# Performance work log

Hardware: AMD Instinct MI355X
Metric: run time of the kernel (lower is better)

The kernel has to match this reference:

```python
import jax, jax.numpy as jnp
import numpy as np

B, T, E, H = 8, 1024, 1024, 16
D = E // H  # head_dim = 64
MAX_OFFSET = 0.5


def setup_inputs() -> dict:
    key = jax.random.key(0)
    ks = jax.random.split(key, 12)
    s = 0.02
    return {
        "query": jax.random.normal(ks[0], (B, T, E), jnp.float32),
        "key_": jax.random.normal(ks[1], (B, T, E), jnp.float32),
        "value": jax.random.normal(ks[2], (B, T, E), jnp.float32),
        "Wq": jax.random.normal(ks[3], (E, E), jnp.float32) * s,
        "bq": jnp.zeros((E,), jnp.float32),
        "Wk": jax.random.normal(ks[4], (E, E), jnp.float32) * s,
        "bk": jnp.zeros((E,), jnp.float32),
        "Wv": jax.random.normal(ks[5], (E, E), jnp.float32) * s,
        "bv": jnp.zeros((E,), jnp.float32),
        "Wo": jax.random.normal(ks[6], (E, E), jnp.float32) * s,
        "bo": jnp.zeros((E,), jnp.float32),
        "bias_table": jax.random.normal(ks[7], (2 * T - 1, H), jnp.float32) * s,
        "offset": jax.random.normal(ks[8], (1,), jnp.float32) * 0.1,
    }


def _temporal_bias(bias_table, offset):
    # relative position index: [T, T] in [0, 2T-2]
    coords = jnp.arange(T)
    rel = (coords[:, None] - coords[None, :]) + (T - 1)
    bounded = jnp.tanh(offset) * MAX_OFFSET  # scalar (shape (1,))
    adj = jnp.clip(rel.astype(jnp.float32) + bounded, 0.0, 2.0 * T - 2.0)
    lo = jnp.floor(adj).astype(jnp.int32)
    hi = jnp.ceil(adj).astype(jnp.int32)
    w = adj - lo.astype(jnp.float32)  # [T, T]
    lo_val = bias_table[lo]  # [T, T, H]
    hi_val = bias_table[hi]  # [T, T, H]
    bias = lo_val * (1.0 - w[..., None]) + hi_val * w[..., None]
    # -> [1, H, T, T]
    return jnp.transpose(bias, (2, 0, 1))[None]


def reference(query, key_, value, Wq, bq, Wk, bk, Wv, bv, Wo, bo, bias_table, offset):
    scale = D ** -0.5
    # torch Linear: x @ W.T + b
    q = (jnp.einsum('bte,fe->btf', query, Wq) + bq).reshape(B, T, H, D).transpose(0, 2, 1, 3)
    k = (jnp.einsum('bte,fe->btf', key_, Wk) + bk).reshape(B, T, H, D).transpose(0, 2, 1, 3)
    v = (jnp.einsum('bte,fe->btf', value, Wv) + bv).reshape(B, T, H, D).transpose(0, 2, 1, 3)
    scores = jnp.einsum('bhqd,bhkd->bhqk', q, k) * scale  # [B, H, T, T]
    scores = scores + _temporal_bias(bias_table, offset)
    attn = jax.nn.softmax(scores, axis=-1)
    out = jnp.einsum('bhqk,bhkd->bhqd', attn, v)  # [B, H, T, D]
    out = out.transpose(0, 2, 1, 3).reshape(B, T, E)
    return jnp.einsum('bte,fe->btf', out, Wo) + bo
```

## Files before the change

### kernel.cpp

```cpp
#include <hip/hip_runtime.h>
#include <hip/hip_bf16.h>
#include <stdint.h>

#define B_ 8
#define T_ 1024
#define E_ 1024
#define H_ 16
#define D_ 64
#define NREL 2047

using bf16 = __hip_bfloat16;
typedef __attribute__((ext_vector_type(8))) short bhalf8;
typedef __attribute__((ext_vector_type(4))) float f32x4;

typedef __attribute__((address_space(3))) uint32_t lds32_t;
typedef const __attribute__((address_space(1))) uint32_t glb32_t;
__device__ __forceinline__ void gld_lds16(const bf16* g, bf16* l) {
  __builtin_amdgcn_global_load_lds((glb32_t*)(const void*)g, (lds32_t*)(void*)l, 16, 0, 0);
}

__device__ __forceinline__ bhalf8 cvt8(const float4 a, const float4 b) {
  bf16 t[8];
  t[0] = __float2bfloat16(a.x); t[1] = __float2bfloat16(a.y);
  t[2] = __float2bfloat16(a.z); t[3] = __float2bfloat16(a.w);
  t[4] = __float2bfloat16(b.x); t[5] = __float2bfloat16(b.y);
  t[6] = __float2bfloat16(b.z); t[7] = __float2bfloat16(b.w);
  return *(const bhalf8*)t;
}

__global__ __launch_bounds__(256) void cvt_w4(const float* __restrict__ Wq,
                                              const float* __restrict__ Wk,
                                              const float* __restrict__ Wv,
                                              const float* __restrict__ Wo,
                                              bf16* __restrict__ d) {
  const int z = blockIdx.y;
  const float* s = (z == 0) ? Wq : (z == 1) ? Wk : (z == 2) ? Wv : Wo;
  const int i = (blockIdx.x * 256 + threadIdx.x) * 8;
  const float4 a = *(const float4*)(s + i);
  const float4 b = *(const float4*)(s + i + 4);
  *(bhalf8*)(d + (size_t)z * E_ * E_ + i) = cvt8(a, b);
}

__global__ void bias_pre(const float* __restrict__ table, const float* __restrict__ offset,
                         float* __restrict__ db) {
  const int idx = blockIdx.x * 256 + threadIdx.x;
  if (idx >= NREL * H_) return;
  const int r = idx >> 4;
  const int h = idx & 15;
  const float bounded = tanhf(offset[0]) * 0.5f;
  float adj = (float)r + bounded;
  adj = fminf(fmaxf(adj, 0.f), 2046.f);
  const int lo = (int)floorf(adj);
  const int hi = (int)ceilf(adj);
  const float wgt = adj - (float)lo;
  const float v = table[lo * H_ + h] * (1.f - wgt) + table[hi * H_ + h] * wgt;
  db[h * NREL + r] = v * 1.4426950408889634f;
}

__global__ __launch_bounds__(256, 3) void gemm_qkv(const float* __restrict__ Xq,
                                                   const float* __restrict__ Xk,
                                                   const float* __restrict__ Xv,
                                                   const bf16* __restrict__ Wc,
                                                   const float* __restrict__ bqp,
                                                   const float* __restrict__ bkp,
                                                   const float* __restrict__ bvp,
                                                   bf16* __restrict__ dst) {
  __shared__ bf16 As[2 * 128 * 32];
  __shared__ bf16 Bs[2 * 128 * 32];
  const int tid = threadIdx.x;
  const int lane = tid & 63;
  const int w = tid >> 6;
  const int quad = lane >> 4;
  const int l15 = lane & 15;
  const int m0 = blockIdx.x * 128;
  const int n0 = blockIdx.y * 128;
  const int z = blockIdx.z;
  const float* A = (z == 0) ? Xq : ((z == 1) ? Xk : Xv);
  const float* bias = (z == 0) ? bqp : ((z == 1) ? bkp : bvp);
  const bf16* W = Wc + (size_t)z * E_ * E_;
  bf16* out = dst + (size_t)z * B_ * T_ * D_ * H_;
  const int wm = (w >> 1) * 64;
  const int wn = (w & 1) * 64;

  const f32x4 zero4 = {0.f, 0.f, 0.f, 0.f};
  f32x4 acc[4][4];
#pragma unroll
  for (int i = 0; i < 4; ++i)
#pragma unroll
    for (int j = 0; j < 4; ++j) acc[i][j] = zero4;

  const int srow = w * 32 + (lane >> 2);
  const int scol = (lane & 3) * 8;
  const float* Ag = A + (size_t)(m0 + srow) * E_ + scol;
  const bf16* Wg = W + (size_t)(n0 + srow) * E_ + scol;
  const int sidx = w * 1024 + lane * 8;

  float4 p0 = *(const float4*)(Ag);
  float4 p1 = *(const float4*)(Ag + 4);
  float4 p2 = *(const float4*)(Ag + (size_t)16 * E_);
  float4 p3 = *(const float4*)(Ag + (size_t)16 * E_ + 4);
  *(bhalf8*)(As + sidx) = cvt8(p0, p1);
  *(bhalf8*)(As + sidx + 512) = cvt8(p2, p3);
  gld_lds16(Wg, Bs + sidx);
  gld_lds16(Wg + (size_t)16 * E_, Bs + sidx + 512);
  p0 = *(const float4*)(Ag + 32);
  p1 = *(const float4*)(Ag + 36);
  p2 = *(const float4*)(Ag + (size_t)16 * E_ + 32);
  p3 = *(const float4*)(Ag + (size_t)16 * E_ + 36);
  __syncthreads();

  for (int kt = 0; kt < 32; ++kt) {
    const int cur = (kt & 1) * 4096;
    bhalf8 af[4], bfr[4];
#pragma unroll
    for (int t2 = 0; t2 < 4; ++t2) {
      af[t2] = *(const bhalf8*)(As + cur + (wm + t2 * 16 + l15) * 32 + quad * 8);
      bfr[t2] = *(const bhalf8*)(Bs + cur + (wn + t2 * 16 + l15) * 32 + quad * 8);
    }
    if (kt < 31) {
      const int nxt = 4096 - cur;
      const int kc = (kt + 1) * 32;
      gld_lds16(Wg + kc, Bs + nxt + sidx);
      gld_lds16(Wg + (size_t)16 * E_ + kc, Bs + nxt + sidx + 512);
      *(bhalf8*)(As + nxt + sidx) = cvt8(p0, p1);
      *(bhalf8*)(As + nxt + sidx + 512) = cvt8(p2, p3);
      if (kt < 30) {
        const int kc2 = kc + 32;
        p0 = *(const float4*)(Ag + kc2);
        p1 = *(const float4*)(Ag + kc2 + 4);
        p2 = *(const float4*)(Ag + (size_t)16 * E_ + kc2);
        p3 = *(const float4*)(Ag + (size_t)16 * E_ + kc2 + 4);
      }
    }
#pragma unroll
    for (int mt = 0; mt < 4; ++mt)
#pragma unroll
      for (int nt = 0; nt < 4; ++nt)
        acc[mt][nt] = __builtin_amdgcn_mfma_f32_16x16x32_bf16(af[mt], bfr[nt], acc[mt][nt], 0, 0, 0);
    __syncthreads();
  }

#pragma unroll
  for (int mt = 0; mt < 4; ++mt) {
#pragma unroll
    for (int nt = 0; nt < 4; ++nt) {
      const int n = n0 + wn + nt * 16 + l15;
      const float bv = bias[n];
#pragma unroll
      for (int r = 0; r < 4; ++r) {
        const int m = m0 + wm + mt * 16 + quad * 4 + r;
        const float v = acc[mt][nt][r] + bv;
        const int bb = m >> 10, tq = m & 1023, hh = n >> 6, d = n & 63;
        out[(((size_t)bb * H_ + hh) * T_ + tq) * D_ + d] = __float2bfloat16(v);
      }
    }
  }
}

template <int SCATTER, int F32OUT>
__global__ __launch_bounds__(256) void gemm_bt(const bf16* __restrict__ A,
                                               const bf16* __restrict__ W,
                                               const float* __restrict__ bias,
                                               void* __restrict__ dst_) {
  __shared__ bf16 As[2 * 128 * 32];
  __shared__ bf16 Bs[2 * 128 * 32];
  const int tid = threadIdx.x;
  const int lane = tid & 63;
  const int w = tid >> 6;
  const int quad = lane >> 4;
  const int l15 = lane & 15;
  const int m0 = blockIdx.x * 128;
  const int n0 = blockIdx.y * 128;
  const int wm = (w >> 1) * 64;
  const int wn = (w & 1) * 64;

  const f32x4 zero4 = {0.f, 0.f, 0.f, 0.f};
  f32x4 acc[4][4];
#pragma unroll
  for (int i = 0; i < 4; ++i)
#pragma unroll
    for (int j = 0; j < 4; ++j) acc[i][j] = zero4;

  const int srow0 = w * 32 + (lane >> 2);
  const int scol = (lane & 3) * 8;
  const bf16* Ag = A + (size_t)(m0 + srow0) * E_ + scol;
  const bf16* Wg = W + (size_t)(n0 + srow0) * E_ + scol;
  const int sidx = w * 1024 + lane * 8;

  gld_lds16(Ag, As + sidx);
  gld_lds16(Ag + (size_t)16 * E_, As + sidx + 512);
  gld_lds16(Wg, Bs + sidx);
  gld_lds16(Wg + (size_t)16 * E_, Bs + sidx + 512);
  __syncthreads();

  for (int kt = 0; kt < 32; ++kt) {
    const int cur = (kt & 1) * 4096;
    bhalf8 af[4], bfr[4];
#pragma unroll
    for (int t = 0; t < 4; ++t) {
      af[t] = *(const bhalf8*)(As + cur + (wm + t * 16 + l15) * 32 + quad * 8);
      bfr[t] = *(const bhalf8*)(Bs + cur + (wn + t * 16 + l15) * 32 + quad * 8);
    }
    if (kt < 31) {
      const int nxt = 4096 - cur;
      const int kc = (kt + 1) * 32;
      gld_lds16(Ag + kc, As + nxt + sidx);
      gld_lds16(Ag + (size_t)16 * E_ + kc, As + nxt + sidx + 512);
      gld_lds16(Wg + kc, Bs + nxt + sidx);
      gld_lds16(Wg + (size_t)16 * E_ + kc, Bs + nxt + sidx + 512);
    }
#pragma unroll
    for (int mt = 0; mt < 4; ++mt)
#pragma unroll
      for (int nt = 0; nt < 4; ++nt)
        acc[mt][nt] = __builtin_amdgcn_mfma_f32_16x16x32_bf16(af[mt], bfr[nt], acc[mt][nt], 0, 0, 0);
    __syncthreads();
  }

#pragma unroll
  for (int mt = 0; mt < 4; ++mt) {
#pragma unroll
    for (int nt = 0; nt < 4; ++nt) {
      const int n = n0 + wn + nt * 16 + l15;
      const float bv = bias[n];
#pragma unroll
      for (int r = 0; r < 4; ++r) {
        const int m = m0 + wm + mt * 16 + quad * 4 + r;
        const float v = acc[mt][nt][r] + bv;
        if (SCATTER) {
          const int bb = m >> 10, t = m & 1023, hh = n >> 6, d = n & 63;
          ((bf16*)dst_)[(((size_t)bb * H_ + hh) * T_ + t) * D_ + d] = __float2bfloat16(v);
        } else if (F32OUT) {
          ((float*)dst_)[(size_t)m * E_ + n] = v;
        } else {
          ((bf16*)dst_)[(size_t)m * E_ + n] = __float2bfloat16(v);
        }
      }
    }
  }
}

__device__ __forceinline__ int ps_off(int row, int colbyte) {
  return row * 128 + (colbyte ^ ((row & 7) << 4));
}

__global__ __launch_bounds__(256, 4) void attn_kernel(const bf16* __restrict__ Q,
                                                      const bf16* __restrict__ K,
                                                      const bf16* __restrict__ V,
                                                      const float* __restrict__ db,
                                                      bf16* __restrict__ xout) {
  const int tid = threadIdx.x;
  const int lane = tid & 63;
  const int w = tid >> 6;
  const int quad = lane >> 4;
  const int l15 = lane & 15;
  const int bh = blockIdx.x;
  const int h = bh & 15;
  const int b = bh >> 4;
  const int q0 = blockIdx.y * 128;

  __shared__ bf16 Vt[64][72];
  __shared__ __align__(16) bf16 Ps[4][32 * 64];
  __shared__ float dbs[1152];

  const size_t base = (size_t)bh * T_ * D_;
  const bf16* Qp = Q + base;
  const bf16* Kp = K + base;
  const bf16* Vp = V + base;
  const float* dbh = db + h * NREL;

  for (int t = tid; t < 1151; t += 256) dbs[t] = dbh[q0 + t];

  const int qw = q0 + w * 32;
  bhalf8 aq[2][2];
#pragma unroll
  for (int mt = 0; mt < 2; ++mt)
#pragma unroll
    for (int ks = 0; ks < 2; ++ks)
      aq[mt][ks] = *(const bhalf8*)(Qp + (size_t)(qw + mt * 16 + l15) * D_ + ks * 32 + quad * 8);

  const f32x4 zero4 = {0.f, 0.f, 0.f, 0.f};
  f32x4 o[2][4];
#pragma unroll
  for (int mt = 0; mt < 2; ++mt)
#pragma unroll
    for (int nt = 0; nt < 4; ++nt) o[mt][nt] = zero4;
  float mrow[2] = {-1e30f, -1e30f};
  float lrow[2] = {0.f, 0.f};

  const int vrow0 = tid >> 3;
  const int vc8 = (tid & 7) * 8;
  bhalf8 vreg[2];
  vreg[0] = *(const bhalf8*)(Vp + (size_t)vrow0 * D_ + vc8);
  vreg[1] = *(const bhalf8*)(Vp + (size_t)(vrow0 + 32) * D_ + vc8);

  char* const psw = (char*)&Ps[w][0];

  for (int it = 0; it < 16; ++it) {
    const int kb = it * 64;
    bhalf8 bk[4][2];
#pragma unroll
    for (int nt = 0; nt < 4; ++nt) {
      const bf16* kr = Kp + (size_t)(kb + nt * 16 + l15) * D_ + quad * 8;
      bk[nt][0] = *(const bhalf8*)kr;
      bk[nt][1] = *(const bhalf8*)(kr + 32);
    }

    __syncthreads();
#pragma unroll
    for (int s = 0; s < 2; ++s) {
      const int row = vrow0 + s * 32;
      const bf16* vp = (const bf16*)&vreg[s];
      const int kvp = (row + vc8) & 63;
#pragma unroll
      for (int j = 0; j < 8; ++j) Vt[vc8 + j][kvp] = vp[j];
    }
    __syncthreads();
    if (it < 15) {
      const int kb2 = kb + 64;
      vreg[0] = *(const bhalf8*)(Vp + (size_t)(kb2 + vrow0) * D_ + vc8);
      vreg[1] = *(const bhalf8*)(Vp + (size_t)(kb2 + vrow0 + 32) * D_ + vc8);
    }

    f32x4 s4[2][4];
    __builtin_amdgcn_s_setprio(1);
#pragma unroll
    for (int nt = 0; nt < 4; ++nt) {
#pragma unroll
      for (int mt = 0; mt < 2; ++mt) {
        f32x4 a = zero4;
        a = __builtin_amdgcn_mfma_f32_16x16x32_bf16(bk[nt][0], aq[mt][0], a, 0, 0, 0);
        a = __builtin_amdgcn_mfma_f32_16x16x32_bf16(bk[nt][1], aq[mt][1], a, 0, 0, 0);
        s4[mt][nt] = a;
      }
    }
    __builtin_amdgcn_s_setprio(0);

#pragma unroll
    for (int mt = 0; mt < 2; ++mt) {
      const int ib = w * 32 + mt * 16 + l15 + 1023 - kb;
      float mnt[4];
#pragma unroll
      for (int nt = 0; nt < 4; ++nt) {
#pragma unroll
        for (int r = 0; r < 4; ++r) {
          const float sv = s4[mt][nt][r] * 0.18033688011112042f + dbs[ib - nt * 16 - quad * 4 - r];
          s4[mt][nt][r] = sv;
        }
        mnt[nt] = fmaxf(fmaxf(s4[mt][nt][0], s4[mt][nt][1]),
                        fmaxf(s4[mt][nt][2], s4[mt][nt][3]));
      }
      float tmx = fmaxf(fmaxf(mnt[0], mnt[1]), fmaxf(mnt[2], mnt[3]));
      tmx = fmaxf(tmx, __shfl_xor(tmx, 16, 64));
      tmx = fmaxf(tmx, __shfl_xor(tmx, 32, 64));
      if (!__all(tmx - mrow[mt] <= 11.0f)) {
        const float mnew = fmaxf(mrow[mt], tmx);
        const float alpha = __builtin_amdgcn_exp2f(mrow[mt] - mnew);
        mrow[mt] = mnew;
        lrow[mt] *= alpha;
#pragma unroll
        for (int nt = 0; nt < 4; ++nt) o[mt][nt] *= alpha;
      }
      const float mcur = mrow[mt];
      float psum[4];
#pragma unroll
      for (int nt = 0; nt < 4; ++nt) {
        float p0 = __builtin_amdgcn_exp2f(s4[mt][nt][0] - mcur);
        float p1 = __builtin_amdgcn_exp2f(s4[mt][nt][1] - mcur);
        float p2 = __builtin_amdgcn_exp2f(s4[mt][nt][2] - mcur);
        float p3 = __builtin_amdgcn_exp2f(s4[mt][nt][3] - mcur);
        s4[mt][nt][0] = p0; s4[mt][nt][1] = p1;
        s4[mt][nt][2] = p2; s4[mt][nt][3] = p3;
        psum[nt] = (p0 + p1) + (p2 + p3);
      }
      float sum = (psum[0] + psum[1]) + (psum[2] + psum[3]);
      sum += __shfl_xor(sum, 16, 64);
      sum += __shfl_xor(sum, 32, 64);
      lrow[mt] += sum;

#pragma unroll
      for (int nt = 0; nt < 4; ++nt) {
        alignas(8) bf16 t4[4];
#pragma unroll
        for (int r = 0; r < 4; ++r) t4[r] = __float2bfloat16(s4[mt][nt][r]);
        *(uint2*)(psw + ps_off(mt * 16 + l15, nt * 32 + quad * 8)) = *(const uint2*)t4;
      }
    }

    bhalf8 pb[2][2];
#pragma unroll
    for (int mt = 0; mt < 2; ++mt)
#pragma unroll
      for (int ks = 0; ks < 2; ++ks)
        pb[mt][ks] = *(const bhalf8*)(psw + ps_off(mt * 16 + l15, ks * 64 + quad * 16));
    const int rot = (l15 >> 3);
    __builtin_amdgcn_s_setprio(1);
#pragma unroll
    for (int nt = 0; nt < 4; ++nt) {
      const int drow = nt * 16 + l15;
#pragma unroll
      for (int ks = 0; ks < 2; ++ks) {
        const int gp = (4 * ks + quad + 2 * nt + rot) & 7;
        const bhalf8 vb = *(const bhalf8*)&Vt[drow][gp * 8];
#pragma unroll
        for (int mt = 0; mt < 2; ++mt)
          o[mt][nt] = __builtin_amdgcn_mfma_f32_16x16x32_bf16(vb, pb[mt][ks], o[mt][nt], 0, 0, 0);
      }
    }
    __builtin_amdgcn_s_setprio(0);
  }

#pragma unroll
  for (int mt = 0; mt < 2; ++mt) {
    const float inv = 1.f / lrow[mt];
#pragma unroll
    for (int nt = 0; nt < 4; ++nt) {
      alignas(8) bf16 t4[4];
#pragma unroll
      for (int r = 0; r < 4; ++r) t4[r] = __float2bfloat16(o[mt][nt][r] * inv);
      *(uint2*)(psw + ps_off(mt * 16 + l15, nt * 32 + quad * 8)) = *(const uint2*)t4;
    }
  }
#pragma unroll
  for (int t = 0; t < 4; ++t) {
    const int idx = t * 64 + lane;
    const int row = idx >> 3;
    const int c = idx & 7;
    const bhalf8 val = *(const bhalf8*)(psw + ps_off(row, c * 16));
    *(bhalf8*)&xout[((size_t)b * T_ + qw + row) * E_ + h * D_ + c * 8] = val;
  }
}

extern "C" void kernel_launch(void* const* d_in, const int* in_sizes, int n_in,
                              void* d_out, int out_size, void* d_ws, size_t ws_size,
                              hipStream_t stream) {
  const float* query = (const float*)d_in[0];
  const float* key_  = (const float*)d_in[1];
  const float* value = (const float*)d_in[2];
  const float* Wq = (const float*)d_in[3];
  const float* bq = (const float*)d_in[4];
  const float* Wk = (const float*)d_in[5];
  const float* bk = (const float*)d_in[6];
  const float* Wv = (const float*)d_in[7];
  const float* bv = (const float*)d_in[8];
  const float* Wo = (const float*)d_in[9];
  const float* bo = (const float*)d_in[10];
  const float* table = (const float*)d_in[11];
  const float* offset = (const float*)d_in[12];
  float* out = (float*)d_out;

  char* ws = (char*)d_ws;
  const size_t ME = (size_t)B_ * T_ * E_;
  const size_t EE = (size_t)E_ * E_;
  float* db = (float*)ws;
  bf16* wc  = (bf16*)(ws + 131072);
  bf16* qb  = wc + 4 * EE;
  bf16* kb  = qb + ME;
  bf16* vb2 = kb + ME;
  bf16* x2  = vb2 + ME;

  dim3 bb(256, 1, 1);
  const int gEE = (int)(EE / 8 / 256);

  bias_pre<<<dim3(128), bb, 0, stream>>>(table, offset, db);
  cvt_w4<<<dim3(gEE, 4), bb, 0, stream>>>(Wq, Wk, Wv, Wo, wc);

  gemm_qkv<<<dim3(64, 8, 3), bb, 0, stream>>>(query, key_, value, wc, bq, bk, bv, qb);

  attn_kernel<<<dim3(128, 8, 1), bb, 0, stream>>>(qb, kb, vb2, db, x2);

  gemm_bt<0, 1><<<dim3(64, 8, 1), bb, 0, stream>>>(x2, wc + 3 * EE, bo, out);
}
```

Baseline: 346.8 us.

## Double-buffer V tile in attention and swizzle GEMM block order for L2 reuse

The attention kernel now keeps two LDS buffers for the transposed V tile. The next V tile is written after the PV MFMAs, which removes one of the two __syncthreads per iteration. The QKV and output GEMMs switch to a 1D grid that is remapped so that groups of 8 M-blocks sweep all N-blocks together, aiming for better L2 reuse of the weight and activation tiles. The extra V buffer raises LDS use per block, which could lower occupancy for the 4-blocks-per-CU launch bound.

```diff
diff --git a/kernel.cpp b/kernel.cpp
--- a/kernel.cpp
+++ b/kernel.cpp
@@ -72,9 +72,11 @@
   const int w = tid >> 6;
   const int quad = lane >> 4;
   const int l15 = lane & 15;
-  const int m0 = blockIdx.x * 128;
-  const int n0 = blockIdx.y * 128;
-  const int z = blockIdx.z;
+  const int nblk = blockIdx.x;
+  const int g = ((nblk >> 6) << 3) | (nblk & 7);
+  const int z = g >> 6;
+  const int m0 = (g & 63) * 128;
+  const int n0 = ((nblk >> 3) & 7) * 128;
   const float* A = (z == 0) ? Xq : ((z == 1) ? Xk : Xv);
   const float* bias = (z == 0) ? bqp : ((z == 1) ? bkp : bvp);
   const bf16* W = Wc + (size_t)z * E_ * E_;
@@ -169,8 +171,10 @@
   const int w = tid >> 6;
   const int quad = lane >> 4;
   const int l15 = lane & 15;
-  const int m0 = blockIdx.x * 128;
-  const int n0 = blockIdx.y * 128;
+  const int nblk = blockIdx.x;
+  const int g = ((nblk >> 6) << 3) | (nblk & 7);
+  const int m0 = g * 128;
+  const int n0 = ((nblk >> 3) & 7) * 128;
   const int wm = (w >> 1) * 64;
   const int wn = (w & 1) * 64;
 
@@ -259,7 +263,7 @@
   const int b = bh >> 4;
   const int q0 = blockIdx.y * 128;
 
-  __shared__ bf16 Vt[64][72];
+  __shared__ bf16 Vt[2][64][72];
   __shared__ __align__(16) bf16 Ps[4][32 * 64];
   __shared__ float dbs[1152];
 
@@ -294,32 +298,31 @@
   vreg[0] = *(const bhalf8*)(Vp + (size_t)vrow0 * D_ + vc8);
   vreg[1] = *(const bhalf8*)(Vp + (size_t)(vrow0 + 32) * D_ + vc8);
 
+#pragma unroll
+  for (int s = 0; s < 2; ++s) {
+    const int row = vrow0 + s * 32;
+    const bf16* vp = (const bf16*)&vreg[s];
+    const int kvp = (row + vc8) & 63;
+#pragma unroll
+    for (int j = 0; j < 8; ++j) Vt[0][vc8 + j][kvp] = vp[j];
+  }
+  __syncthreads();
+  vreg[0] = *(const bhalf8*)(Vp + (size_t)(64 + vrow0) * D_ + vc8);
+  vreg[1] = *(const bhalf8*)(Vp + (size_t)(64 + vrow0 + 32) * D_ + vc8);
+
   char* const psw = (char*)&Ps[w][0];
+  const int rot = (l15 >> 3);
 
   for (int it = 0; it < 16; ++it) {
     const int kb = it * 64;
+    const int cur = it & 1;
+
     bhalf8 bk[4][2];
 #pragma unroll
     for (int nt = 0; nt < 4; ++nt) {
       const bf16* kr = Kp + (size_t)(kb + nt * 16 + l15) * D_ + quad * 8;
       bk[nt][0] = *(const bhalf8*)kr;
       bk[nt][1] = *(const bhalf8*)(kr + 32);
-    }
-
-    __syncthreads();
-#pragma unroll
-    for (int s = 0; s < 2; ++s) {
-      const int row = vrow0 + s * 32;
-      const bf16* vp = (const bf16*)&vreg[s];
-      const int kvp = (row + vc8) & 63;
-#pragma unroll
-      for (int j = 0; j < 8; ++j) Vt[vc8 + j][kvp] = vp[j];
-    }
-    __syncthreads();
-    if (it < 15) {
-      const int kb2 = kb + 64;
-      vreg[0] = *(const bhalf8*)(Vp + (size_t)(kb2 + vrow0) * D_ + vc8);
-      vreg[1] = *(const bhalf8*)(Vp + (size_t)(kb2 + vrow0 + 32) * D_ + vc8);
     }
 
     f32x4 s4[2][4];
@@ -393,7 +396,6 @@
 #pragma unroll
       for (int ks = 0; ks < 2; ++ks)
         pb[mt][ks] = *(const bhalf8*)(psw + ps_off(mt * 16 + l15, ks * 64 + quad * 16));
-    const int rot = (l15 >> 3);
     __builtin_amdgcn_s_setprio(1);
 #pragma unroll
     for (int nt = 0; nt < 4; ++nt) {
@@ -401,13 +403,30 @@
 #pragma unroll
       for (int ks = 0; ks < 2; ++ks) {
         const int gp = (4 * ks + quad + 2 * nt + rot) & 7;
-        const bhalf8 vb = *(const bhalf8*)&Vt[drow][gp * 8];
+        const bhalf8 vb = *(const bhalf8*)&Vt[cur][drow][gp * 8];
 #pragma unroll
         for (int mt = 0; mt < 2; ++mt)
           o[mt][nt] = __builtin_amdgcn_mfma_f32_16x16x32_bf16(vb, pb[mt][ks], o[mt][nt], 0, 0, 0);
       }
     }
     __builtin_amdgcn_s_setprio(0);
+
+    if (it < 15) {
+#pragma unroll
+      for (int s = 0; s < 2; ++s) {
+        const int row = vrow0 + s * 32;
+        const bf16* vp = (const bf16*)&vreg[s];
+        const int kvp = (row + vc8) & 63;
+#pragma unroll
+        for (int j = 0; j < 8; ++j) Vt[cur ^ 1][vc8 + j][kvp] = vp[j];
+      }
+      if (it < 14) {
+        const int kb2 = kb + 128;
+        vreg[0] = *(const bhalf8*)(Vp + (size_t)(kb2 + vrow0) * D_ + vc8);
+        vreg[1] = *(const bhalf8*)(Vp + (size_t)(kb2 + vrow0 + 32) * D_ + vc8);
+      }
+    }
+    __syncthreads();
   }
 
 #pragma unroll
@@ -465,9 +484,9 @@
   bias_pre<<<dim3(128), bb, 0, stream>>>(table, offset, db);
   cvt_w4<<<dim3(gEE, 4), bb, 0, stream>>>(Wq, Wk, Wv, Wo, wc);
 
-  gemm_qkv<<<dim3(64, 8, 3), bb, 0, stream>>>(query, key_, value, wc, bq, bk, bv, qb);
+  gemm_qkv<<<dim3(1536), bb, 0, stream>>>(query, key_, value, wc, bq, bk, bv, qb);
 
   attn_kernel<<<dim3(128, 8, 1), bb, 0, stream>>>(qb, kb, vb2, db, x2);
 
-  gemm_bt<0, 1><<<dim3(64, 8, 1), bb, 0, stream>>>(x2, wc + 3 * EE, bo, out);
-}
+  gemm_bt<0, 1><<<dim3(512), bb, 0, stream>>>(x2, wc + 3 * EE, bo, out);
+}
```

After: 376.8 us. 8.7% more time.
